# Performance work log

Hardware: AMD Instinct MI355X
Metric: run time of the kernel (lower is better)

## Reference

```python
import jax, jax.numpy as jnp
import numpy as np

N_NODES = 50000
N_EDGES = 400000
N_GRAPHS = 64
D_IN = 200
D_HID = 32
N_CLASS = 2


def setup_inputs() -> dict:
    key = jax.random.key(0)
    ks = jax.random.split(key, 16)
    x = jax.random.normal(ks[0], (N_NODES, D_IN), dtype=jnp.float32)
    edge_index = jax.random.randint(ks[1], (2, N_EDGES), 0, N_NODES, dtype=jnp.int64)
    edge_attr = jax.random.normal(ks[2], (N_EDGES,), dtype=jnp.float32)
    batch = jnp.sort(jax.random.randint(ks[3], (N_NODES,), 0, N_GRAPHS, dtype=jnp.int64))
    s = 0.05
    params = dict(
        W1r=jax.random.normal(ks[4], (D_IN, D_HID), jnp.float32) * s,
        W1l=jax.random.normal(ks[5], (D_IN, D_HID), jnp.float32) * s,
        b1=jnp.zeros((D_HID,), jnp.float32),
        W2r=jax.random.normal(ks[6], (D_HID, D_HID), jnp.float32) * s,
        W2l=jax.random.normal(ks[7], (D_HID, D_HID), jnp.float32) * s,
        b2=jnp.zeros((D_HID,), jnp.float32),
        W3r=jax.random.normal(ks[8], (D_HID, D_HID), jnp.float32) * s,
        W3l=jax.random.normal(ks[9], (D_HID, D_HID), jnp.float32) * s,
        b3=jnp.zeros((D_HID,), jnp.float32),
        Wlin=jax.random.normal(ks[10], (D_HID, N_CLASS), jnp.float32) * s,
        blin=jnp.zeros((N_CLASS,), jnp.float32),
    )
    return dict(x=x, edge_index=edge_index, edge_attr=edge_attr, batch=batch, **params)


def _graph_conv(x, src, dst, Wr, Wl, b):
    # PyG GraphConv: out_i = lin_rel(sum_{j->i} x_j) + lin_root(x_i)
    agg = jax.ops.segment_sum(x[src], dst, num_segments=x.shape[0])  # [N, d_in]
    return agg @ Wr + b + x @ Wl


def reference(x, edge_index, edge_attr, batch,
              W1r, W1l, b1, W2r, W2l, b2, W3r, W3l, b3, Wlin, blin):
    src, dst = edge_index[0], edge_index[1]
    # dropout is identity at inference (training=False)
    h = jax.nn.elu(_graph_conv(x, src, dst, W1r, W1l, b1))
    h = jax.nn.elu(_graph_conv(h, src, dst, W2r, W2l, b2))
    h = jax.nn.elu(_graph_conv(h, src, dst, W3r, W3l, b3))
    # global mean pool over graphs
    sums = jax.ops.segment_sum(h, batch, num_segments=N_GRAPHS)  # [G, d]
    counts = jax.ops.segment_sum(jnp.ones((h.shape[0],), h.dtype), batch,
                                 num_segments=N_GRAPHS)
    pooled = sums / jnp.maximum(counts, 1.0)[:, None]
    logits = pooled @ Wlin + blin
    return jax.nn.log_softmax(logits, axis=1)
```

## Files before the change

### kernel.cpp

```cpp
#include <hip/hip_runtime.h>
#include <hip/hip_bf16.h>


#define D_IN 200
#define N_GRAPHS 64

#define KP 232
#define KB 7
#define WT_ELEMS (64 * KP)
#define W23_ELEMS 2048
#define MAXDEG 32

#define NT 256
#define HS_STR 40

typedef __attribute__((ext_vector_type(8))) short bf16x8;
typedef __attribute__((ext_vector_type(4))) float f32x4;

__device__ __forceinline__ float4 elu4(float4 v) {
    float4 o;
    o.x = (v.x > 0.f) ? v.x : expm1f(v.x);
    o.y = (v.y > 0.f) ? v.y : expm1f(v.y);
    o.z = (v.z > 0.f) ? v.z : expm1f(v.z);
    o.w = (v.w > 0.f) ? v.w : expm1f(v.w);
    return o;
}

__global__ __launch_bounds__(NT) void k1(const float* __restrict__ X,
                                         const float* __restrict__ W1r,
                                         const float* __restrict__ W1l,
                                         const float* __restrict__ W2r,
                                         const float* __restrict__ W2l,
                                         const float* __restrict__ W3r,
                                         const float* __restrict__ W3l,
                                         const int* __restrict__ src,
                                         const int* __restrict__ dst,
                                         int* __restrict__ cnt,
                                         int* __restrict__ colIdx,
                                         __hip_bfloat16* __restrict__ Wt2,
                                         __hip_bfloat16* __restrict__ Wt3,
                                         __hip_bfloat16* __restrict__ yr16,
                                         float* __restrict__ yl,
                                         int N, int E, int t64, int egrid) {
    __shared__ __hip_bfloat16 WtS[WT_ELEMS];
    int tid = threadIdx.x, blk = blockIdx.x;
    if (blk < t64) {
        for (int idx = tid; idx < WT_ELEMS; idx += NT) {
            int n = idx / KP, k = idx - n * KP;
            float v = 0.f;
            if (k < D_IN) v = (n < 32) ? W1r[k * 32 + n] : W1l[k * 32 + (n - 32)];
            WtS[idx] = __float2bfloat16(v);
        }
        __syncthreads();
        int lane = tid & 63, wv = tid >> 6;
        int l15 = lane & 15, q = lane >> 4;
        long base = (long)blk * 64;
        long row = base + wv * 16 + l15;
        long rowc = (row < (long)N) ? row : (long)(N - 1);
        const float* xr = X + rowc * D_IN;
        bf16x8 a[KB];
#pragma unroll
        for (int kb = 0; kb < KB; ++kb) {
            int k0 = kb * 32 + q * 8;
            union { __hip_bfloat16 h[8]; bf16x8 v; } u;
            if (k0 + 8 <= D_IN) {
                float4 v0 = *(const float4*)(xr + k0);
                float4 v1 = *(const float4*)(xr + k0 + 4);
                u.h[0] = __float2bfloat16(v0.x); u.h[1] = __float2bfloat16(v0.y);
                u.h[2] = __float2bfloat16(v0.z); u.h[3] = __float2bfloat16(v0.w);
                u.h[4] = __float2bfloat16(v1.x); u.h[5] = __float2bfloat16(v1.y);
                u.h[6] = __float2bfloat16(v1.z); u.h[7] = __float2bfloat16(v1.w);
            } else {
#pragma unroll
                for (int j = 0; j < 8; ++j) {
                    int k = k0 + j;
                    u.h[j] = __float2bfloat16(k < D_IN ? xr[k] : 0.f);
                }
            }
            a[kb] = u.v;
        }
#pragma unroll
        for (int ns = 0; ns < 4; ++ns) {
            f32x4 acc = {0.f, 0.f, 0.f, 0.f};
#pragma unroll
            for (int kb = 0; kb < KB; ++kb) {
                bf16x8 bfrag = *(const bf16x8*)(const void*)
                    (WtS + (ns * 16 + l15) * KP + kb * 32 + q * 8);
                acc = __builtin_amdgcn_mfma_f32_16x16x32_bf16(a[kb], bfrag, acc, 0, 0, 0);
            }
            int col = ns * 16 + l15;
#pragma unroll
            for (int r = 0; r < 4; ++r) {
                long node = base + wv * 16 + q * 4 + r;
                if (node < N) {
                    if (col < 32) yr16[node * 32 + col] = __float2bfloat16(acc[r]);
                    else          yl[node * 32 + (col - 32)] = acc[r];
                }
            }
        }
    } else if (blk < t64 + egrid) {
        int e = (blk - t64) * NT + tid;
        if (e < E) {
            int d = dst[e];
            int r = atomicAdd(&cnt[d], 1);
            if (r < MAXDEG)
                colIdx[(long)r * N + d] = src[e];
        }
    } else {
        int idx = (blk - t64 - egrid) * NT + tid;
        if (idx < 2 * W23_ELEMS) {
            int which = idx >> 11;
            int j = idx & 2047;
            int n = j >> 5, k = j & 31;
            const float* Wr = which ? W3r : W2r;
            const float* Wl = which ? W3l : W2l;
            float v = (n < 32) ? Wr[k * 32 + n] : Wl[k * 32 + (n - 32)];
            (which ? Wt3 : Wt2)[j] = __float2bfloat16(v);
        }
    }
}

__device__ __forceinline__ void agg_node8(const __hip_bfloat16* __restrict__ yr16,
                                          const float* __restrict__ yl,
                                          const int* __restrict__ cnt,
                                          const int* __restrict__ colIdx,
                                          const float* __restrict__ b,
                                          int node, int ln, int half, int N,
                                          float4& oA, float4& oB) {
    const uint4* yv = (const uint4*)yr16;
    int deg = cnt[node]; deg = (deg < MAXDEG) ? deg : MAXDEG;
    int f0 = ln * 8;
    float4 bA = *(const float4*)(b + f0);
    float4 bB = *(const float4*)(b + f0 + 4);
    float4 rA = *(const float4*)(yl + (long)node * 32 + f0);
    float4 rB = *(const float4*)(yl + (long)node * 32 + f0 + 4);
    float acc[8] = {0.f, 0.f, 0.f, 0.f, 0.f, 0.f, 0.f, 0.f};
    for (int p0 = half; p0 < deg; p0 += 16) {
        int jj[8]; float m[8];
#pragma unroll
        for (int i = 0; i < 8; ++i) {
            int pi = p0 + 2 * i;
            m[i] = (pi < deg) ? 1.f : 0.f;
            pi = (pi < deg) ? pi : (deg - 1);
            jj[i] = colIdx[(long)pi * N + node];
        }
        uint4 v[8];
#pragma unroll
        for (int i = 0; i < 8; ++i) v[i] = yv[(long)jj[i] * 4 + ln];
#pragma unroll
        for (int i = 0; i < 8; ++i) {
            uint d0 = v[i].x, d1 = v[i].y, d2 = v[i].z, d3 = v[i].w;
            acc[0] = fmaf(__uint_as_float(d0 << 16),          m[i], acc[0]);
            acc[1] = fmaf(__uint_as_float(d0 & 0xffff0000u),  m[i], acc[1]);
            acc[2] = fmaf(__uint_as_float(d1 << 16),          m[i], acc[2]);
            acc[3] = fmaf(__uint_as_float(d1 & 0xffff0000u),  m[i], acc[3]);
            acc[4] = fmaf(__uint_as_float(d2 << 16),          m[i], acc[4]);
            acc[5] = fmaf(__uint_as_float(d2 & 0xffff0000u),  m[i], acc[5]);
            acc[6] = fmaf(__uint_as_float(d3 << 16),          m[i], acc[6]);
            acc[7] = fmaf(__uint_as_float(d3 & 0xffff0000u),  m[i], acc[7]);
        }
    }
#pragma unroll
    for (int t = 0; t < 8; ++t) acc[t] += __shfl_xor(acc[t], 4);
    oA = elu4(make_float4(acc[0] + bA.x + rA.x, acc[1] + bA.y + rA.y,
                          acc[2] + bA.z + rA.z, acc[3] + bA.w + rA.w));
    oB = elu4(make_float4(acc[4] + bB.x + rB.x, acc[5] + bB.y + rB.y,
                          acc[6] + bB.z + rB.z, acc[7] + bB.w + rB.w));
}

__global__ __launch_bounds__(NT) void agg_gemm_mfma(
        const __hip_bfloat16* __restrict__ yr16_in, const float* __restrict__ yl_in,
        const int* __restrict__ cnt, const int* __restrict__ colIdx,
        const float* __restrict__ b, const __hip_bfloat16* __restrict__ Wt2,
        __hip_bfloat16* __restrict__ yr16_out, float* __restrict__ yl_out, int N) {
    __shared__ __hip_bfloat16 hs[32 * HS_STR];
    int tid = threadIdx.x;
    int ln = tid & 3, half = (tid >> 2) & 1, nl = tid >> 3;
    long base = (long)blockIdx.x * 32;
    int node = (int)base + nl;
    int nodec = (node < N) ? node : (N - 1);
    float4 oA, oB;
    agg_node8(yr16_in, yl_in, cnt, colIdx, b, nodec, ln, half, N, oA, oB);
    union { __hip_bfloat16 h[8]; float4 v; } u;
    if (node < N) {
        u.h[0] = __float2bfloat16(oA.x); u.h[1] = __float2bfloat16(oA.y);
        u.h[2] = __float2bfloat16(oA.z); u.h[3] = __float2bfloat16(oA.w);
        u.h[4] = __float2bfloat16(oB.x); u.h[5] = __float2bfloat16(oB.y);
        u.h[6] = __float2bfloat16(oB.z); u.h[7] = __float2bfloat16(oB.w);
    } else {
        u.v = make_float4(0.f, 0.f, 0.f, 0.f);
    }
    if (half == 0)
        *(float4*)(&hs[nl * HS_STR + ln * 8]) = u.v;
    __syncthreads();

    int lane = tid & 63, w = tid >> 6;
    int l15 = lane & 15, q = lane >> 4;
    int rg = w & 1, cg = w >> 1;
    bf16x8 a = *(const bf16x8*)(const void*)(&hs[(rg * 16 + l15) * HS_STR + q * 8]);
#pragma unroll
    for (int s = 0; s < 2; ++s) {
        int ns = cg * 2 + s;
        f32x4 acc = {0.f, 0.f, 0.f, 0.f};
        bf16x8 bfrag = *(const bf16x8*)(const void*)(Wt2 + (ns * 16 + l15) * 32 + q * 8);
        acc = __builtin_amdgcn_mfma_f32_16x16x32_bf16(a, bfrag, acc, 0, 0, 0);
        int col = ns * 16 + l15;
#pragma unroll
        for (int r = 0; r < 4; ++r) {
            long nd = base + rg * 16 + q * 4 + r;
            if (nd < N) {
                if (col < 32) yr16_out[nd * 32 + col] = __float2bfloat16(acc[r]);
                else          yl_out[nd * 32 + (col - 32)] = acc[r];
            }
        }
    }
}

__global__ __launch_bounds__(NT) void agg_elu_k(const __hip_bfloat16* __restrict__ yr16,
                                                const float* __restrict__ yl,
                                                const int* __restrict__ cnt,
                                                const int* __restrict__ colIdx,
                                                const float* __restrict__ b,
                                                float* __restrict__ hout, int N) {
    int tid = threadIdx.x;
    int ln = tid & 3, half = (tid >> 2) & 1;
    int node = blockIdx.x * 32 + (tid >> 3);
    int nodec = (node < N) ? node : (N - 1);
    float4 oA, oB;
    agg_node8(yr16, yl, cnt, colIdx, b, nodec, ln, half, N, oA, oB);
    if (half == 0 && node < N) {
        int f0 = ln * 8;
        *(float4*)(hout + (long)node * 32 + f0) = oA;
        *(float4*)(hout + (long)node * 32 + f0 + 4) = oB;
    }
}

__global__ __launch_bounds__(NT) void pool_head(const float4* __restrict__ h4,
                                                const int* __restrict__ batch,
                                                const float* __restrict__ Wlin,
                                                const float* __restrict__ blin,
                                                float* __restrict__ out, int N) {
    int g = blockIdx.x;
    int lo = 0, hi = N;
    while (lo < hi) { int mid = (lo + hi) >> 1; if (batch[mid] < g) lo = mid + 1; else hi = mid; }
    int start = lo;
    hi = N;
    while (lo < hi) { int mid = (lo + hi) >> 1; if (batch[mid] < g + 1) lo = mid + 1; else hi = mid; }
    int end = lo;

    int f4 = threadIdx.x & 7, r = threadIdx.x >> 3;
    float4 acc = make_float4(0.f, 0.f, 0.f, 0.f);
    for (int i = start + r; i < end; i += 32) {
        float4 v = h4[(long)i * 8 + f4];
        acc.x += v.x; acc.y += v.y; acc.z += v.z; acc.w += v.w;
    }
    __shared__ float4 red[32][8];
    __shared__ float pooledS[32];
    red[r][f4] = acc;
    __syncthreads();
    if (r == 0) {
        float4 s = make_float4(0.f, 0.f, 0.f, 0.f);
#pragma unroll
        for (int r2 = 0; r2 < 32; ++r2) {
            float4 v = red[r2][f4];
            s.x += v.x; s.y += v.y; s.z += v.z; s.w += v.w;
        }
        float inv = 1.f / fmaxf((float)(end - start), 1.f);
        pooledS[f4 * 4 + 0] = s.x * inv;
        pooledS[f4 * 4 + 1] = s.y * inv;
        pooledS[f4 * 4 + 2] = s.z * inv;
        pooledS[f4 * 4 + 3] = s.w * inv;
    }
    __syncthreads();
    if (threadIdx.x == 0) {
        float c0 = blin[0], c1 = blin[1];
        for (int k = 0; k < 32; ++k) {
            float pk = pooledS[k];
            c0 += pk * Wlin[k * 2 + 0];
            c1 += pk * Wlin[k * 2 + 1];
        }
        float m = fmaxf(c0, c1);
        float lse = m + logf(expf(c0 - m) + expf(c1 - m));
        out[g * 2 + 0] = c0 - lse;
        out[g * 2 + 1] = c1 - lse;
    }
}

extern "C" void kernel_launch(void* const* d_in, const int* in_sizes, int n_in,
                              void* d_out, int out_size, void* d_ws, size_t ws_size,
                              hipStream_t stream) {
    const float* x     = (const float*)d_in[0];
    const int*   eidx  = (const int*)d_in[1];
    const int*   batch = (const int*)d_in[3];
    const float* W1r = (const float*)d_in[4];
    const float* W1l = (const float*)d_in[5];
    const float* b1  = (const float*)d_in[6];
    const float* W2r = (const float*)d_in[7];
    const float* W2l = (const float*)d_in[8];
    const float* b2  = (const float*)d_in[9];
    const float* W3r = (const float*)d_in[10];
    const float* W3l = (const float*)d_in[11];
    const float* b3  = (const float*)d_in[12];
    const float* Wlin = (const float*)d_in[13];
    const float* blin = (const float*)d_in[14];
    float* out = (float*)d_out;

    const int N = in_sizes[0] / D_IN;
    const int E = in_sizes[1] / 2;
    const int* src = eidx;
    const int* dst = eidx + E;

    char* w = (char*)d_ws;
    auto alloc = [&](size_t bytes) -> void* {
        void* p = (void*)w;
        w += (bytes + 255) & ~(size_t)255;
        return p;
    };
    int* cnt     = (int*)alloc((size_t)N * 4);
    int* colIdx  = (int*)alloc((size_t)N * MAXDEG * 4);
    __hip_bfloat16* Wt2   = (__hip_bfloat16*)alloc((size_t)W23_ELEMS * 2);
    __hip_bfloat16* Wt3   = (__hip_bfloat16*)alloc((size_t)W23_ELEMS * 2);
    __hip_bfloat16* yr16A = (__hip_bfloat16*)alloc((size_t)N * 32 * 2);
    __hip_bfloat16* yr16B = (__hip_bfloat16*)alloc((size_t)N * 32 * 2);
    float* ylA = (float*)alloc((size_t)N * 32 * 4);
    float* ylB = (float*)alloc((size_t)N * 32 * 4);
    float* hA  = (float*)alloc((size_t)N * 32 * 4);

    hipMemsetAsync(cnt, 0, (size_t)N * 4, stream);

    int egrid = (E + NT - 1) / NT;
    int w23g  = (2 * W23_ELEMS + NT - 1) / NT;
    int t64   = (N + 63) / 64;
    int g32   = (N + 31) / 32;

    k1<<<t64 + egrid + w23g, NT, 0, stream>>>(
        x, W1r, W1l, W2r, W2l, W3r, W3l, src, dst, cnt, colIdx,
        Wt2, Wt3, yr16A, ylA, N, E, t64, egrid);
    agg_gemm_mfma<<<g32, NT, 0, stream>>>(yr16A, ylA, cnt, colIdx, b1, Wt2,
                                          yr16B, ylB, N);
    agg_gemm_mfma<<<g32, NT, 0, stream>>>(yr16B, ylB, cnt, colIdx, b2, Wt3,
                                          yr16A, ylA, N);
    agg_elu_k<<<g32, NT, 0, stream>>>(yr16A, ylA, cnt, colIdx, b3, hA, N);
    pool_head<<<N_GRAPHS, NT, 0, stream>>>((const float4*)hA, batch, Wlin, blin, out, N);
}
```

Before: 190.1 us.

## Split fused first-layer kernel into edge-count/weight-pack and separate GEMM

The first kernel used to do three jobs in one launch: per-block LDS transposition of W1 plus the layer-1 GEMM, CSR-like edge bucketing with atomics, and W2/W3 packing. Now a count_pack kernel handles edge bucketing and packs W1 once into a global bf16 buffer, and a separate gemm1 kernel reads B fragments straight from global/L2 instead of rebuilding the transposed W1 in LDS in every block. This removes the redundant per-block weight conversion and the LDS footprint, but adds a kernel launch and serialises the atomic edge pass before the GEMM instead of overlapping them.

```diff
diff --git a/kernel.cpp b/kernel.cpp
--- a/kernel.cpp
+++ b/kernel.cpp
@@ -26,35 +26,62 @@
     return o;
 }
 
-__global__ __launch_bounds__(NT) void k1(const float* __restrict__ X,
-                                         const float* __restrict__ W1r,
-                                         const float* __restrict__ W1l,
-                                         const float* __restrict__ W2r,
-                                         const float* __restrict__ W2l,
-                                         const float* __restrict__ W3r,
-                                         const float* __restrict__ W3l,
-                                         const int* __restrict__ src,
-                                         const int* __restrict__ dst,
-                                         int* __restrict__ cnt,
-                                         int* __restrict__ colIdx,
-                                         __hip_bfloat16* __restrict__ Wt2,
-                                         __hip_bfloat16* __restrict__ Wt3,
-                                         __hip_bfloat16* __restrict__ yr16,
-                                         float* __restrict__ yl,
-                                         int N, int E, int t64, int egrid) {
-    __shared__ __hip_bfloat16 WtS[WT_ELEMS];
-    int tid = threadIdx.x, blk = blockIdx.x;
-    if (blk < t64) {
-        for (int idx = tid; idx < WT_ELEMS; idx += NT) {
-            int n = idx / KP, k = idx - n * KP;
+__global__ __launch_bounds__(NT) void count_pack(const int* __restrict__ src,
+                                                 const int* __restrict__ dst,
+                                                 int* __restrict__ cnt,
+                                                 int* __restrict__ colIdx,
+                                                 int E, int N,
+                                                 const float* __restrict__ W1r,
+                                                 const float* __restrict__ W1l,
+                                                 const float* __restrict__ W2r,
+                                                 const float* __restrict__ W2l,
+                                                 const float* __restrict__ W3r,
+                                                 const float* __restrict__ W3l,
+                                                 __hip_bfloat16* __restrict__ Wt,
+                                                 __hip_bfloat16* __restrict__ Wt2,
+                                                 __hip_bfloat16* __restrict__ Wt3,
+                                                 int egrid, int wgrid) {
+    int blk = blockIdx.x;
+    if (blk < egrid) {
+        int e = blk * NT + threadIdx.x;
+        if (e < E) {
+            int d = dst[e];
+            int r = atomicAdd(&cnt[d], 1);
+            if (r < MAXDEG)
+                colIdx[(long)r * N + d] = src[e];
+        }
+    } else if (blk < egrid + wgrid) {
+        int idx = (blk - egrid) * NT + threadIdx.x;
+        if (idx < WT_ELEMS) {
+            int n = idx / KP, k = idx % KP;
             float v = 0.f;
             if (k < D_IN) v = (n < 32) ? W1r[k * 32 + n] : W1l[k * 32 + (n - 32)];
-            WtS[idx] = __float2bfloat16(v);
-        }
-        __syncthreads();
-        int lane = tid & 63, wv = tid >> 6;
-        int l15 = lane & 15, q = lane >> 4;
-        long base = (long)blk * 64;
+            Wt[idx] = __float2bfloat16(v);
+        }
+    } else {
+        int idx = (blk - egrid - wgrid) * NT + threadIdx.x;
+        if (idx < 2 * W23_ELEMS) {
+            int which = idx >> 11;
+            int j = idx & 2047;
+            int n = j >> 5, k = j & 31;
+            const float* Wr = which ? W3r : W2r;
+            const float* Wl = which ? W3l : W2l;
+            float v = (n < 32) ? Wr[k * 32 + n] : Wl[k * 32 + (n - 32)];
+            (which ? Wt3 : Wt2)[j] = __float2bfloat16(v);
+        }
+    }
+}
+
+__global__ __launch_bounds__(NT) void gemm1(const float* __restrict__ X,
+                                            const __hip_bfloat16* __restrict__ Wt,
+                                            __hip_bfloat16* __restrict__ yr16,
+                                            float* __restrict__ yl, int N) {
+    int tid = threadIdx.x, bid = blockIdx.x, nb = gridDim.x;
+    int lane = tid & 63, wv = tid >> 6;
+    int l15 = lane & 15, q = lane >> 4;
+    int ntile = (N + 63) >> 6;
+    for (int tile = bid; tile < ntile; tile += nb) {
+        long base = (long)tile * 64;
         long row = base + wv * 16 + l15;
         long rowc = (row < (long)N) ? row : (long)(N - 1);
         const float* xr = X + rowc * D_IN;
@@ -85,7 +112,7 @@
 #pragma unroll
             for (int kb = 0; kb < KB; ++kb) {
                 bf16x8 bfrag = *(const bf16x8*)(const void*)
-                    (WtS + (ns * 16 + l15) * KP + kb * 32 + q * 8);
+                    (Wt + (ns * 16 + l15) * KP + kb * 32 + q * 8);
                 acc = __builtin_amdgcn_mfma_f32_16x16x32_bf16(a[kb], bfrag, acc, 0, 0, 0);
             }
             int col = ns * 16 + l15;
@@ -97,25 +124,6 @@
                     else          yl[node * 32 + (col - 32)] = acc[r];
                 }
             }
-        }
-    } else if (blk < t64 + egrid) {
-        int e = (blk - t64) * NT + tid;
-        if (e < E) {
-            int d = dst[e];
-            int r = atomicAdd(&cnt[d], 1);
-            if (r < MAXDEG)
-                colIdx[(long)r * N + d] = src[e];
-        }
-    } else {
-        int idx = (blk - t64 - egrid) * NT + tid;
-        if (idx < 2 * W23_ELEMS) {
-            int which = idx >> 11;
-            int j = idx & 2047;
-            int n = j >> 5, k = j & 31;
-            const float* Wr = which ? W3r : W2r;
-            const float* Wl = which ? W3l : W2l;
-            float v = (n < 32) ? Wr[k * 32 + n] : Wl[k * 32 + (n - 32)];
-            (which ? Wt3 : Wt2)[j] = __float2bfloat16(v);
         }
     }
 }
@@ -318,6 +326,7 @@
     };
     int* cnt     = (int*)alloc((size_t)N * 4);
     int* colIdx  = (int*)alloc((size_t)N * MAXDEG * 4);
+    __hip_bfloat16* Wt    = (__hip_bfloat16*)alloc((size_t)WT_ELEMS * 2);
     __hip_bfloat16* Wt2   = (__hip_bfloat16*)alloc((size_t)W23_ELEMS * 2);
     __hip_bfloat16* Wt3   = (__hip_bfloat16*)alloc((size_t)W23_ELEMS * 2);
     __hip_bfloat16* yr16A = (__hip_bfloat16*)alloc((size_t)N * 32 * 2);
@@ -329,13 +338,15 @@
     hipMemsetAsync(cnt, 0, (size_t)N * 4, stream);
 
     int egrid = (E + NT - 1) / NT;
+    int wgrid = (WT_ELEMS + NT - 1) / NT;
     int w23g  = (2 * W23_ELEMS + NT - 1) / NT;
     int t64   = (N + 63) / 64;
     int g32   = (N + 31) / 32;
 
-    k1<<<t64 + egrid + w23g, NT, 0, stream>>>(
-        x, W1r, W1l, W2r, W2l, W3r, W3l, src, dst, cnt, colIdx,
-        Wt2, Wt3, yr16A, ylA, N, E, t64, egrid);
+    count_pack<<<egrid + wgrid + w23g, NT, 0, stream>>>(
+        src, dst, cnt, colIdx, E, N, W1r, W1l, W2r, W2l, W3r, W3l,
+        Wt, Wt2, Wt3, egrid, wgrid);
+    gemm1<<<t64, NT, 0, stream>>>(x, Wt, yr16A, ylA, N);
     agg_gemm_mfma<<<g32, NT, 0, stream>>>(yr16A, ylA, cnt, colIdx, b1, Wt2,
                                           yr16B, ylB, N);
     agg_gemm_mfma<<<g32, NT, 0, stream>>>(yr16B, ylB, cnt, colIdx, b2, Wt3,
```

New measurement: 185.2 us. 1.03x faster.
